# Performance work log

Hardware: AMD Instinct MI355X
Metric: run time of the kernel (lower is better)

## Reference

```python
import jax, jax.numpy as jnp
import numpy as np

B, N, G = 32, 262144, 256


def setup_inputs() -> dict:
    key = jax.random.key(0)
    k1, k2, k3 = jax.random.split(key, 3)
    pr = jax.random.normal(k1, (B, N), dtype=jnp.float32)
    inp_means = jax.random.normal(k2, (B, G), dtype=jnp.float32)
    vr = jax.random.randint(k3, (B, N, 1), 0, G, dtype=jnp.int32)
    W = jnp.ones((2,), dtype=jnp.float32)  # hist_weight, ones initializer
    return {"pr": pr, "inp_means": inp_means, "vr": vr, "W": W}


def reference(pr, inp_means, vr, W):
    sg = jax.lax.stop_gradient
    G = inp_means.shape[1]
    v = jnp.squeeze(vr, -1)  # [B, N] int cluster ids (stop_gradient in orig; int anyway)
    p_sg = sg(pr)

    # Per-batch segmented min/max/sum/any over clusters (replaces python loop over g).
    def seg(p, psg, vi):
        mn = jnp.full((G,), jnp.inf, p.dtype).at[vi].min(psg)    # min(where(gidx, pr, inf))
        mx = jnp.full((G,), -jnp.inf, p.dtype).at[vi].max(psg)   # max(where(gidx, pr, -inf))
        sm = jnp.zeros((G,), p.dtype).at[vi].add(p)              # sum(where(gidx, pr, 0))
        any_ = jnp.zeros((G,), bool).at[vi].set(True)            # reduce_any(gidx)
        return mn, mx, sm, any_

    vmins, vmaxs, vsum, vany = jax.vmap(seg)(pr, p_sg, v)  # each [B, G]
    # Original divides sum by cast(any)->1.0 (or 0/0=nan -> 0), i.e. the group SUM.
    vmeans = jnp.where(vany, vsum, jnp.zeros((), pr.dtype))
    vmeans = (inp_means * W[0] + vmeans * W[1]) / (W[0] + W[1])

    no_scale = vmins == vmaxs  # [B, G]
    vmins_g = jnp.take_along_axis(jnp.where(no_scale, 0.0, vmins), v, axis=1)  # [B, N]
    vmaxs_g = jnp.take_along_axis(jnp.where(no_scale, 1.0, vmaxs), v, axis=1)  # [B, N]

    sort_ids = jnp.argsort(vmeans, axis=1)
    orig_ids = jnp.argsort(sort_ids, axis=1)  # inverse permutation
    vs = jnp.take_along_axis(vmeans, sort_ids, axis=1)  # [B, G]
    cd = jnp.concatenate([vs[:, :1], vs, vs[:, -1:] * 2], axis=1)  # [B, G+2]
    # conv1d with kernel ones(2)/c, VALID: out[i] = (cd[i] + cd[i+1]) / c
    f0 = (cd[:, :-2] + cd[:, 1:-1]) / 1.999  # conv(...)[:, :-1]
    f1 = (cd[:, 1:-1] + cd[:, 2:]) / 2.001   # conv(...)[:, 1:]
    f0 = jnp.take_along_axis(
        jnp.where(no_scale, 0.0, jnp.take_along_axis(f0, orig_ids, axis=1)), v, axis=1)
    f1 = jnp.take_along_axis(
        jnp.where(no_scale, 1.0, jnp.take_along_axis(f1, orig_ids, axis=1)), v, axis=1)

    tmp = (sg(pr) - sg(vmins_g)) / sg(vmaxs_g - vmins_g) * (f1 - f0) + f0  # [B, N]
    bad = jnp.isnan(tmp) | (tmp == 0.0)
    s = pr / jnp.where(bad, 1.0, tmp)  # safe denominator (grad-safe)
    scale = jnp.where(bad | jnp.isnan(s) | jnp.isinf(s), 0.0, s)
    return pr * scale
```

## Files before the change

kernel.cpp:

```cpp
#include <hip/hip_runtime.h>
#include <math.h>

#define NB 32
#define NN 262144
#define NG 256
#define NC 64
#define CH (NN/NC)
#define SC (CH/4)
#define CD 64
#define ELD (NN/CD)

__global__ __launch_bounds__(256) void k_count(const int* __restrict__ vr,
                                               unsigned long long* __restrict__ wcnt16,
                                               unsigned* __restrict__ gid32){
  __shared__ unsigned sc[4][NG];
  const int t    = threadIdx.x;
  const int lane = t & 63;
  const int w    = t >> 6;
  sc[0][t] = 0u; sc[1][t] = 0u; sc[2][t] = 0u; sc[3][t] = 0u;
  __syncthreads();

  const int b = blockIdx.x / NC;
  const int c = blockIdx.x % NC;
  const size_t base = (size_t)b*NN + (size_t)c*CH;
  const int4* v4 = (const int4*)(vr + base);

#pragma unroll
  for (int i = 0; i < 4; i++){
    int idx = w*256 + i*64 + lane;
    int4 v = v4[idx];
    atomicAdd(&sc[w][v.x], 1u);
    atomicAdd(&sc[w][v.y], 1u);
    atomicAdd(&sc[w][v.z], 1u);
    atomicAdd(&sc[w][v.w], 1u);
    gid32[(base >> 2) + idx] =
      (unsigned)v.x | ((unsigned)v.y << 8) | ((unsigned)v.z << 16) | ((unsigned)v.w << 24);
  }
  __syncthreads();

  unsigned c0 = sc[0][t], c1 = sc[1][t], c2 = sc[2][t], c3 = sc[3][t];
  const size_t cb = (size_t)b*NC + c;
  wcnt16[cb*NG + t] = (unsigned long long)c0
                    | ((unsigned long long)c1 << 16)
                    | ((unsigned long long)c2 << 32)
                    | ((unsigned long long)c3 << 48);
}

__global__ __launch_bounds__(256) void k_offsets(const unsigned long long* __restrict__ wcnt16,
                                                 unsigned* __restrict__ off,
                                                 unsigned* __restrict__ grpbase,
                                                 unsigned* __restrict__ grplen){
  const int b = blockIdx.x;
  const int g = threadIdx.x;

  unsigned v[NC];
#pragma unroll
  for (int c = 0; c < NC; c++){
    unsigned long long x = wcnt16[(size_t)(b*NC + c)*NG + g];
    unsigned lo = (unsigned)x, hi = (unsigned)(x >> 32);
    v[c] = (lo & 0xFFFFu) + (lo >> 16) + (hi & 0xFFFFu) + (hi >> 16);
  }
  unsigned tot = 0;
#pragma unroll
  for (int c = 0; c < NC; c++) tot += v[c];

  __shared__ unsigned ss[NG];
  ss[g] = tot; __syncthreads();
  for (int d = 1; d < NG; d <<= 1){
    unsigned x = (g >= d) ? ss[g - d] : 0u;
    __syncthreads();
    ss[g] += x;
    __syncthreads();
  }
  unsigned base = ss[g] - tot;

  unsigned run = base;
#pragma unroll
  for (int c = 0; c < NC; c++){
    off[(size_t)(b*NC + c)*NG + g] = run;
    run += v[c];
  }
  grpbase[b*NG + g] = base;
  grplen [b*NG + g] = tot;
}

__global__ __launch_bounds__(256) void k_scatter(const float* __restrict__ pr,
                                                 const unsigned* __restrict__ gid32,
                                                 const unsigned* __restrict__ off,
                                                 const unsigned long long* __restrict__ wcnt16,
                                                 float* __restrict__ sorted){
  __shared__ float vbuf[CH];
  __shared__ unsigned char gbuf[CH];
  __shared__ unsigned wcnt[4][NG];
  __shared__ unsigned bias[NG];
  __shared__ unsigned wsum[4];
  const int t    = threadIdx.x;
  const int lane = t & 63;
  const int w    = t >> 6;
  const int b = blockIdx.x / NC;
  const int c = blockIdx.x % NC;
  const size_t base = (size_t)b*NN + (size_t)c*CH;
  const size_t cb   = (size_t)b*NC + c;

  {
    unsigned long long x = wcnt16[cb*NG + t];
    unsigned offt = off[cb*NG + t];
    unsigned lo = (unsigned)x, hi = (unsigned)(x >> 32);
    unsigned w0 = lo & 0xFFFFu, w1 = lo >> 16, w2 = hi & 0xFFFFu, w3 = hi >> 16;
    unsigned tot = w0 + w1 + w2 + w3;

    unsigned v = tot;
#pragma unroll
    for (int d = 1; d < 64; d <<= 1){
      unsigned y = __shfl_up(v, d, 64);
      if (lane >= d) v += y;
    }
    if (lane == 63) wsum[w] = v;
    __syncthreads();
    unsigned pre = 0;
#pragma unroll
    for (int k = 0; k < 3; k++) if (k < w) pre += wsum[k];
    unsigned lb = pre + v - tot;
    wcnt[0][t] = lb;
    wcnt[1][t] = lb + w0;
    wcnt[2][t] = lb + w0 + w1;
    wcnt[3][t] = lb + w0 + w1 + w2;
    bias[t] = offt - lb;
  }
  __syncthreads();

  {
    const unsigned long long below = (lane == 0) ? 0ull : ((1ull << lane) - 1ull);
    const float*    psrc = pr    + base        + (size_t)w*SC;
    const unsigned* gsrc = gid32 + (base >> 2) + (size_t)w*(SC/4);
    const int shft = (lane & 3) * 8;

    float pv[16]; unsigned pk[16];
#pragma unroll
    for (int s = 0; s < 16; s++){
      pv[s] = psrc[s*64 + lane];
      pk[s] = gsrc[s*16 + (lane >> 2)];
    }
#pragma unroll
    for (int s = 0; s < 16; s++){
      int g = (int)((pk[s] >> shft) & 255u);
      unsigned long long mask = ~0ull;
#pragma unroll
      for (int bit = 0; bit < 8; bit++){
        int bv = (g >> bit) & 1;
        unsigned long long bal = __ballot(bv);
        mask &= bv ? bal : ~bal;
      }
      int rank = __popcll(mask & below);
      unsigned old = wcnt[w][g];
      if (rank == 0) wcnt[w][g] = old + (unsigned)__popcll(mask);
      vbuf[old + (unsigned)rank] = pv[s];
      gbuf[old + (unsigned)rank] = (unsigned char)g;
    }
  }
  __syncthreads();

  {
    float* dst = sorted + (size_t)b*NN;
    const unsigned* gbuf32 = (const unsigned*)gbuf;
#pragma unroll
    for (int k = 0; k < CH/256; k++){
      int p = k*256 + t;
      unsigned packed = gbuf32[p >> 2];
      unsigned g = (packed >> ((p & 3) * 8)) & 255u;
      dst[bias[g] + (unsigned)p] = vbuf[p];
    }
  }
}

__global__ __launch_bounds__(32) void k_sum(const float* __restrict__ sorted,
                                            const unsigned* __restrict__ grpbase,
                                            const unsigned* __restrict__ grplen,
                                            float* __restrict__ gsum,
                                            float* __restrict__ gmn,
                                            float* __restrict__ gmx){
  const int lane = threadIdx.x;
  const int b = blockIdx.x >> 3;
  const int g = ((blockIdx.x & 7) << 5) + lane;

  const unsigned base = grpbase[b*NG + g];
  const unsigned len  = grplen [b*NG + g];
  const float* sp = sorted + (size_t)b*NN + base;

  float s = 0.0f, mn = INFINITY, mx = -INFINITY;

  unsigned head = (4u - ((unsigned)(((size_t)sp) >> 2) & 3u)) & 3u;
  if (head > len) head = len;
  for (unsigned i = 0; i < head; i++){
    float v = sp[i];
    s = __fadd_rn(s, v); mn = fminf(mn, v); mx = fmaxf(mx, v);
  }
  const float4* f4 = (const float4*)(sp + head);
  const unsigned rem   = len - head;
  const unsigned nfull = rem >> 4;

  float4 b0[4], b1[4], b2[4], b3[4], b4[4], b5[4], b6[4], b7[4];
#define LOADV(D, K) { D[0]=f4[(K)*4+0]; D[1]=f4[(K)*4+1]; D[2]=f4[(K)*4+2]; D[3]=f4[(K)*4+3]; }
#define CONS1(V)    { s=__fadd_rn(s,(V)); mn=fminf(mn,(V)); mx=fmaxf(mx,(V)); }
#define CONSV(D)    { _Pragma("unroll") for (int j = 0; j < 4; j++){ float4 q = D[j]; \
                      CONS1(q.x) CONS1(q.y) CONS1(q.z) CONS1(q.w) } }

  if (nfull > 0) LOADV(b0, 0)
  if (nfull > 1) LOADV(b1, 1)
  if (nfull > 2) LOADV(b2, 2)
  if (nfull > 3) LOADV(b3, 3)
  if (nfull > 4) LOADV(b4, 4)
  if (nfull > 5) LOADV(b5, 5)
  if (nfull > 6) LOADV(b6, 6)
  if (nfull > 7) LOADV(b7, 7)
  unsigned k = 0;
  for (; k + 8 <= nfull; k += 8){
    CONSV(b0) if (k +  8 < nfull) LOADV(b0, k +  8)
    CONSV(b1) if (k +  9 < nfull) LOADV(b1, k +  9)
    CONSV(b2) if (k + 10 < nfull) LOADV(b2, k + 10)
    CONSV(b3) if (k + 11 < nfull) LOADV(b3, k + 11)
    CONSV(b4) if (k + 12 < nfull) LOADV(b4, k + 12)
    CONSV(b5) if (k + 13 < nfull) LOADV(b5, k + 13)
    CONSV(b6) if (k + 14 < nfull) LOADV(b6, k + 14)
    CONSV(b7) if (k + 15 < nfull) LOADV(b7, k + 15)
  }
  {
    unsigned r = nfull - k;
    if (r > 0) CONSV(b0)
    if (r > 1) CONSV(b1)
    if (r > 2) CONSV(b2)
    if (r > 3) CONSV(b3)
    if (r > 4) CONSV(b4)
    if (r > 5) CONSV(b5)
    if (r > 6) CONSV(b6)
  }
  for (unsigned i = head + (nfull << 4); i < len; i++){
    float v = sp[i];
    s = __fadd_rn(s, v); mn = fminf(mn, v); mx = fmaxf(mx, v);
  }
#undef LOADV
#undef CONS1
#undef CONSV

  gsum[b*NG + g] = s;
  gmn [b*NG + g] = mn;
  gmx [b*NG + g] = mx;
}

__global__ __launch_bounds__(256) void k_pipeline(const float* __restrict__ gsum,
                                                  const float* __restrict__ gmn,
                                                  const float* __restrict__ gmx,
                                                  const float* __restrict__ inp_means,
                                                  const float* __restrict__ Wv,
                                                  float* __restrict__ params){
  const int b = blockIdx.x;
  const int g = threadIdx.x;
  __shared__ float vm[NG];
  __shared__ float vs[NG];

  const float s   = gsum[b*NG + g];
  const float mnf = gmn [b*NG + g];
  const float mxf = gmx [b*NG + g];
  const float W0 = Wv[0], W1 = Wv[1];
  float mean = __fdiv_rn(__fadd_rn(__fmul_rn(inp_means[b*NG + g], W0),
                                   __fmul_rn(s, W1)),
                         __fadd_rn(W0, W1));
  vm[g] = mean;
  __syncthreads();

  int r = 0;
  for (int j = 0; j < NG; j++){
    float x = vm[j];
    r += (x < mean) || (x == mean && j < g);
  }
  vs[r] = mean;
  __syncthreads();

  float c0 = (r == 0)    ? vs[0]                     : vs[r-1];
  float c1 = vs[r];
  float c2 = (r == NG-1) ? __fmul_rn(vs[NG-1], 2.0f) : vs[r+1];
  float f0 = __fdiv_rn(__fadd_rn(c0, c1), 1.999f);
  float f1 = __fdiv_rn(__fadd_rn(c1, c2), 2.001f);

  bool ns = (mnf == mxf);
  params[(b*4 + 0)*NG + g] = ns ? 0.0f : mnf;
  params[(b*4 + 1)*NG + g] = ns ? 1.0f : __fsub_rn(mxf, mnf);
  params[(b*4 + 2)*NG + g] = ns ? 1.0f : __fsub_rn(f1, f0);
  params[(b*4 + 3)*NG + g] = ns ? 0.0f : f0;
}

static __device__ __forceinline__ float apply_one(float p, unsigned g,
                                                  const float* __restrict__ sp0,
                                                  const float* __restrict__ sp1,
                                                  const float* __restrict__ sp2,
                                                  const float* __restrict__ sp3){
  float t1  = __fsub_rn(p, sp0[g]);
  float t3  = __fdiv_rn(t1, sp1[g]);
  float t5  = __fmul_rn(t3, sp2[g]);
  float tmp = __fadd_rn(t5, sp3[g]);
  bool bad = __builtin_isnan(tmp) || (tmp == 0.0f);
  float s = __fdiv_rn(p, bad ? 1.0f : tmp);
  bool bad2 = bad || __builtin_isnan(s) || __builtin_isinf(s);
  float sc = bad2 ? 0.0f : s;
  return __fmul_rn(p, sc);
}

__global__ __launch_bounds__(256) void k_apply(const float* __restrict__ pr,
                                               const unsigned* __restrict__ gid32,
                                               const float* __restrict__ params,
                                               float* __restrict__ out){
  __shared__ float sp0[NG], sp1[NG], sp2[NG], sp3[NG];
  const int t = threadIdx.x;
  const int b = blockIdx.x / CD;
  const int c = blockIdx.x % CD;

  sp0[t] = params[(b*4 + 0)*NG + t];
  sp1[t] = params[(b*4 + 1)*NG + t];
  sp2[t] = params[(b*4 + 2)*NG + t];
  sp3[t] = params[(b*4 + 3)*NG + t];
  __syncthreads();

  const size_t base = (size_t)b*NN + (size_t)c*ELD;
  const float4* p4 = (const float4*)(pr + base);
  float4* o4 = (float4*)(out + base);

#pragma unroll
  for (int i = 0; i < ELD/1024; i++){
    float4 p = p4[i*256 + t];
    unsigned pk = gid32[(base >> 2) + i*256 + t];
    float4 r;
    r.x = apply_one(p.x,  pk        & 255u, sp0, sp1, sp2, sp3);
    r.y = apply_one(p.y, (pk >>  8) & 255u, sp0, sp1, sp2, sp3);
    r.z = apply_one(p.z, (pk >> 16) & 255u, sp0, sp1, sp2, sp3);
    r.w = apply_one(p.w,  pk >> 24,         sp0, sp1, sp2, sp3);
    o4[i*256 + t] = r;
  }
}

extern "C" void kernel_launch(void* const* d_in, const int* in_sizes, int n_in,
                              void* d_out, int out_size, void* d_ws, size_t ws_size,
                              hipStream_t stream){
  const float* pr        = (const float*)d_in[0];
  const float* inp_means = (const float*)d_in[1];
  const int*   vr        = (const int*)d_in[2];
  const float* W         = (const float*)d_in[3];
  float* out = (float*)d_out;

  char* ws = (char*)d_ws;
  size_t o = 0;
  unsigned long long* wcnt16 = (unsigned long long*)(ws + o); o += (size_t)NB*NC*NG*8;
  unsigned* off     = (unsigned*)(ws + o); o += (size_t)NB*NC*NG*4;
  unsigned* gid32   = (unsigned*)(ws + o); o += (size_t)NB*NN;
  unsigned* grpbase = (unsigned*)(ws + o); o += (size_t)NB*NG*4;
  unsigned* grplen  = (unsigned*)(ws + o); o += (size_t)NB*NG*4;
  float*    gsum    = (float*)   (ws + o); o += (size_t)NB*NG*4;
  float*    gmn     = (float*)   (ws + o); o += (size_t)NB*NG*4;
  float*    gmx     = (float*)   (ws + o); o += (size_t)NB*NG*4;
  float*    params  = (float*)   (ws + o); o += (size_t)NB*NG*16;
  float* sorted = out;

  k_count   <<<NB*NC, 256, 0, stream>>>(vr, wcnt16, gid32);
  k_offsets <<<NB,     NG, 0, stream>>>(wcnt16, off, grpbase, grplen);
  k_scatter <<<NB*NC, 256, 0, stream>>>(pr, gid32, off, wcnt16, sorted);
  k_sum     <<<NB*8,   32, 0, stream>>>(sorted, grpbase, grplen, gsum, gmn, gmx);
  k_pipeline<<<NB,     NG, 0, stream>>>(gsum, gmn, gmx, inp_means, W, params);
  k_apply   <<<NB*CD, 256, 0, stream>>>(pr, gid32, params, out);
}
```

Measured before the change: 173.0 us.

## Double chunk count, wave-shuffle scan in offsets, derive group bounds from offsets

Doubles the number of chunks per batch, so the count and scatter kernels launch twice as many blocks, each holding half the data and a smaller shared buffer. k_offsets drops the 64-entry register array and the shared-memory Hillis-Steele scan. It uses a wavefront shuffle scan and re-reads the counts on the second pass. k_sum now derives group base and length from the first chunk's offsets, so the grpbase/grplen arrays go away. The price is twice the per-chunk count and offset traffic and twice the length of the serial loop over chunks in k_offsets.

```diff
diff --git a/kernel.cpp b/kernel.cpp
--- a/kernel.cpp
+++ b/kernel.cpp
@@ -4,15 +4,15 @@
 #define NB 32
 #define NN 262144
 #define NG 256
-#define NC 64
+#define NC 128
 #define CH (NN/NC)
 #define SC (CH/4)
 #define CD 64
 #define ELD (NN/CD)
 
-__global__ __launch_bounds__(256) void k_count(const int* __restrict__ vr,
-                                               unsigned long long* __restrict__ wcnt16,
-                                               unsigned* __restrict__ gid32){
+__global__ __launch_bounds__(256, 8) void k_count(const int* __restrict__ vr,
+                                                  unsigned long long* __restrict__ wcnt16,
+                                                  unsigned* __restrict__ gid32){
   __shared__ unsigned sc[4][NG];
   const int t    = threadIdx.x;
   const int lane = t & 63;
@@ -26,8 +26,8 @@
   const int4* v4 = (const int4*)(vr + base);
 
 #pragma unroll
-  for (int i = 0; i < 4; i++){
-    int idx = w*256 + i*64 + lane;
+  for (int i = 0; i < 2; i++){
+    int idx = w*128 + i*64 + lane;
     int4 v = v4[idx];
     atomicAdd(&sc[w][v.x], 1u);
     atomicAdd(&sc[w][v.y], 1u);
@@ -47,48 +47,50 @@
 }
 
 __global__ __launch_bounds__(256) void k_offsets(const unsigned long long* __restrict__ wcnt16,
-                                                 unsigned* __restrict__ off,
-                                                 unsigned* __restrict__ grpbase,
-                                                 unsigned* __restrict__ grplen){
+                                                 unsigned* __restrict__ off){
   const int b = blockIdx.x;
   const int g = threadIdx.x;
-
-  unsigned v[NC];
-#pragma unroll
+  const int lane = g & 63;
+  const int w    = g >> 6;
+  __shared__ unsigned wsum[4];
+
+  const unsigned long long* src = wcnt16 + (size_t)b*NC*NG + g;
+  unsigned tot = 0;
+#pragma unroll 8
   for (int c = 0; c < NC; c++){
-    unsigned long long x = wcnt16[(size_t)(b*NC + c)*NG + g];
+    unsigned long long x = src[(size_t)c*NG];
     unsigned lo = (unsigned)x, hi = (unsigned)(x >> 32);
-    v[c] = (lo & 0xFFFFu) + (lo >> 16) + (hi & 0xFFFFu) + (hi >> 16);
-  }
-  unsigned tot = 0;
-#pragma unroll
-  for (int c = 0; c < NC; c++) tot += v[c];
-
-  __shared__ unsigned ss[NG];
-  ss[g] = tot; __syncthreads();
-  for (int d = 1; d < NG; d <<= 1){
-    unsigned x = (g >= d) ? ss[g - d] : 0u;
-    __syncthreads();
-    ss[g] += x;
-    __syncthreads();
-  }
-  unsigned base = ss[g] - tot;
-
-  unsigned run = base;
-#pragma unroll
+    tot += (lo & 0xFFFFu) + (lo >> 16) + (hi & 0xFFFFu) + (hi >> 16);
+  }
+
+  unsigned vscan = tot;
+#pragma unroll
+  for (int d = 1; d < 64; d <<= 1){
+    unsigned y = __shfl_up(vscan, d, 64);
+    if (lane >= d) vscan += y;
+  }
+  if (lane == 63) wsum[w] = vscan;
+  __syncthreads();
+  unsigned pre = 0;
+#pragma unroll
+  for (int k = 0; k < 3; k++) if (k < w) pre += wsum[k];
+
+  unsigned run = pre + vscan - tot;
+  unsigned* dst = off + (size_t)b*NC*NG + g;
+#pragma unroll 8
   for (int c = 0; c < NC; c++){
-    off[(size_t)(b*NC + c)*NG + g] = run;
-    run += v[c];
-  }
-  grpbase[b*NG + g] = base;
-  grplen [b*NG + g] = tot;
-}
-
-__global__ __launch_bounds__(256) void k_scatter(const float* __restrict__ pr,
-                                                 const unsigned* __restrict__ gid32,
-                                                 const unsigned* __restrict__ off,
-                                                 const unsigned long long* __restrict__ wcnt16,
-                                                 float* __restrict__ sorted){
+    dst[(size_t)c*NG] = run;
+    unsigned long long x = src[(size_t)c*NG];
+    unsigned lo = (unsigned)x, hi = (unsigned)(x >> 32);
+    run += (lo & 0xFFFFu) + (lo >> 16) + (hi & 0xFFFFu) + (hi >> 16);
+  }
+}
+
+__global__ __launch_bounds__(256, 8) void k_scatter(const float* __restrict__ pr,
+                                                    const unsigned* __restrict__ gid32,
+                                                    const unsigned* __restrict__ off,
+                                                    const unsigned long long* __restrict__ wcnt16,
+                                                    float* __restrict__ sorted){
   __shared__ float vbuf[CH];
   __shared__ unsigned char gbuf[CH];
   __shared__ unsigned wcnt[4][NG];
@@ -135,14 +137,14 @@
     const unsigned* gsrc = gid32 + (base >> 2) + (size_t)w*(SC/4);
     const int shft = (lane & 3) * 8;
 
-    float pv[16]; unsigned pk[16];
-#pragma unroll
-    for (int s = 0; s < 16; s++){
+    float pv[8]; unsigned pk[8];
+#pragma unroll
+    for (int s = 0; s < 8; s++){
       pv[s] = psrc[s*64 + lane];
       pk[s] = gsrc[s*16 + (lane >> 2)];
     }
 #pragma unroll
-    for (int s = 0; s < 16; s++){
+    for (int s = 0; s < 8; s++){
       int g = (int)((pk[s] >> shft) & 255u);
       unsigned long long mask = ~0ull;
 #pragma unroll
@@ -174,8 +176,7 @@
 }
 
 __global__ __launch_bounds__(32) void k_sum(const float* __restrict__ sorted,
-                                            const unsigned* __restrict__ grpbase,
-                                            const unsigned* __restrict__ grplen,
+                                            const unsigned* __restrict__ off,
                                             float* __restrict__ gsum,
                                             float* __restrict__ gmn,
                                             float* __restrict__ gmx){
@@ -183,8 +184,10 @@
   const int b = blockIdx.x >> 3;
   const int g = ((blockIdx.x & 7) << 5) + lane;
 
-  const unsigned base = grpbase[b*NG + g];
-  const unsigned len  = grplen [b*NG + g];
+  const unsigned* ob = off + (size_t)b*NC*NG;
+  const unsigned base = ob[g];
+  const unsigned nxt  = (g == NG-1) ? (unsigned)NN : ob[g + 1];
+  const unsigned len  = nxt - base;
   const float* sp = sorted + (size_t)b*NN + base;
 
   float s = 0.0f, mn = INFINITY, mx = -INFINITY;
@@ -305,10 +308,10 @@
   return __fmul_rn(p, sc);
 }
 
-__global__ __launch_bounds__(256) void k_apply(const float* __restrict__ pr,
-                                               const unsigned* __restrict__ gid32,
-                                               const float* __restrict__ params,
-                                               float* __restrict__ out){
+__global__ __launch_bounds__(256, 8) void k_apply(const float* __restrict__ pr,
+                                                  const unsigned* __restrict__ gid32,
+                                                  const float* __restrict__ params,
+                                                  float* __restrict__ out){
   __shared__ float sp0[NG], sp1[NG], sp2[NG], sp3[NG];
   const int t = threadIdx.x;
   const int b = blockIdx.x / CD;
@@ -351,8 +354,6 @@
   unsigned long long* wcnt16 = (unsigned long long*)(ws + o); o += (size_t)NB*NC*NG*8;
   unsigned* off     = (unsigned*)(ws + o); o += (size_t)NB*NC*NG*4;
   unsigned* gid32   = (unsigned*)(ws + o); o += (size_t)NB*NN;
-  unsigned* grpbase = (unsigned*)(ws + o); o += (size_t)NB*NG*4;
-  unsigned* grplen  = (unsigned*)(ws + o); o += (size_t)NB*NG*4;
   float*    gsum    = (float*)   (ws + o); o += (size_t)NB*NG*4;
   float*    gmn     = (float*)   (ws + o); o += (size_t)NB*NG*4;
   float*    gmx     = (float*)   (ws + o); o += (size_t)NB*NG*4;
@@ -360,9 +361,9 @@
   float* sorted = out;
 
   k_count   <<<NB*NC, 256, 0, stream>>>(vr, wcnt16, gid32);
-  k_offsets <<<NB,     NG, 0, stream>>>(wcnt16, off, grpbase, grplen);
+  k_offsets <<<NB,    256, 0, stream>>>(wcnt16, off);
   k_scatter <<<NB*NC, 256, 0, stream>>>(pr, gid32, off, wcnt16, sorted);
-  k_sum     <<<NB*8,   32, 0, stream>>>(sorted, grpbase, grplen, gsum, gmn, gmx);
-  k_pipeline<<<NB,     NG, 0, stream>>>(gsum, gmn, gmx, inp_means, W, params);
+  k_sum     <<<NB*8,   32, 0, stream>>>(sorted, off, gsum, gmn, gmx);
+  k_pipeline<<<NB,    256, 0, stream>>>(gsum, gmn, gmx, inp_means, W, params);
   k_apply   <<<NB*CD, 256, 0, stream>>>(pr, gid32, params, out);
 }
```

New measurement: 177.7 us. 2.7% more time.

## Fuse offset prefix computation into scatter kernel, dropping k_offsets launch

Applied to the files above, without the earlier changes.

Removes the separate k_offsets kernel. Each scatter block now reads all 64 chunk counts for its batch, computes per-group totals and the prefix of earlier chunks itself, and derives its global offsets. This saves one kernel launch and the round trip of the off array through memory. In exchange, every scatter block does redundant reads of the batch count table (64x256 64-bit words per block), which should mostly hit L2.

```diff
diff --git a/kernel.cpp b/kernel.cpp
--- a/kernel.cpp
+++ b/kernel.cpp
@@ -46,86 +46,65 @@
                     | ((unsigned long long)c3 << 48);
 }
 
-__global__ __launch_bounds__(256) void k_offsets(const unsigned long long* __restrict__ wcnt16,
-                                                 unsigned* __restrict__ off,
+__global__ __launch_bounds__(256) void k_scatter(const float* __restrict__ pr,
+                                                 const unsigned* __restrict__ gid32,
+                                                 const unsigned long long* __restrict__ wcnt16,
+                                                 float* __restrict__ sorted,
                                                  unsigned* __restrict__ grpbase,
                                                  unsigned* __restrict__ grplen){
-  const int b = blockIdx.x;
-  const int g = threadIdx.x;
-
-  unsigned v[NC];
-#pragma unroll
-  for (int c = 0; c < NC; c++){
-    unsigned long long x = wcnt16[(size_t)(b*NC + c)*NG + g];
-    unsigned lo = (unsigned)x, hi = (unsigned)(x >> 32);
-    v[c] = (lo & 0xFFFFu) + (lo >> 16) + (hi & 0xFFFFu) + (hi >> 16);
-  }
-  unsigned tot = 0;
-#pragma unroll
-  for (int c = 0; c < NC; c++) tot += v[c];
-
-  __shared__ unsigned ss[NG];
-  ss[g] = tot; __syncthreads();
-  for (int d = 1; d < NG; d <<= 1){
-    unsigned x = (g >= d) ? ss[g - d] : 0u;
-    __syncthreads();
-    ss[g] += x;
-    __syncthreads();
-  }
-  unsigned base = ss[g] - tot;
-
-  unsigned run = base;
-#pragma unroll
-  for (int c = 0; c < NC; c++){
-    off[(size_t)(b*NC + c)*NG + g] = run;
-    run += v[c];
-  }
-  grpbase[b*NG + g] = base;
-  grplen [b*NG + g] = tot;
-}
-
-__global__ __launch_bounds__(256) void k_scatter(const float* __restrict__ pr,
-                                                 const unsigned* __restrict__ gid32,
-                                                 const unsigned* __restrict__ off,
-                                                 const unsigned long long* __restrict__ wcnt16,
-                                                 float* __restrict__ sorted){
   __shared__ float vbuf[CH];
   __shared__ unsigned char gbuf[CH];
   __shared__ unsigned wcnt[4][NG];
   __shared__ unsigned bias[NG];
-  __shared__ unsigned wsum[4];
+  __shared__ unsigned wsumA[4];
+  __shared__ unsigned wsumO[4];
   const int t    = threadIdx.x;
   const int lane = t & 63;
   const int w    = t >> 6;
   const int b = blockIdx.x / NC;
   const int c = blockIdx.x % NC;
   const size_t base = (size_t)b*NN + (size_t)c*CH;
-  const size_t cb   = (size_t)b*NC + c;
 
   {
-    unsigned long long x = wcnt16[cb*NG + t];
-    unsigned offt = off[cb*NG + t];
-    unsigned lo = (unsigned)x, hi = (unsigned)(x >> 32);
+    const unsigned long long* tab = wcnt16 + (size_t)b*NC*NG + t;
+    unsigned long long own = 0;
+    unsigned tot_all = 0, tot_before = 0;
+#pragma unroll 8
+    for (int cc = 0; cc < NC; cc++){
+      unsigned long long x = tab[(size_t)cc*NG];
+      unsigned lo = (unsigned)x, hi = (unsigned)(x >> 32);
+      unsigned tt = (lo & 0xFFFFu) + (lo >> 16) + (hi & 0xFFFFu) + (hi >> 16);
+      tot_all += tt;
+      if (cc < c)  tot_before += tt;
+      if (cc == c) own = x;
+    }
+    unsigned lo = (unsigned)own, hi = (unsigned)(own >> 32);
     unsigned w0 = lo & 0xFFFFu, w1 = lo >> 16, w2 = hi & 0xFFFFu, w3 = hi >> 16;
-    unsigned tot = w0 + w1 + w2 + w3;
-
-    unsigned v = tot;
+    unsigned tot_own = w0 + w1 + w2 + w3;
+
+    unsigned va = tot_all, vo = tot_own;
 #pragma unroll
     for (int d = 1; d < 64; d <<= 1){
-      unsigned y = __shfl_up(v, d, 64);
-      if (lane >= d) v += y;
-    }
-    if (lane == 63) wsum[w] = v;
+      unsigned ya = __shfl_up(va, d, 64);
+      unsigned yo = __shfl_up(vo, d, 64);
+      if (lane >= d){ va += ya; vo += yo; }
+    }
+    if (lane == 63){ wsumA[w] = va; wsumO[w] = vo; }
     __syncthreads();
-    unsigned pre = 0;
-#pragma unroll
-    for (int k = 0; k < 3; k++) if (k < w) pre += wsum[k];
-    unsigned lb = pre + v - tot;
+    unsigned preA = 0, preO = 0;
+#pragma unroll
+    for (int k = 0; k < 3; k++) if (k < w){ preA += wsumA[k]; preO += wsumO[k]; }
+    unsigned base_g = preA + va - tot_all;
+    unsigned lb     = preO + vo - tot_own;
     wcnt[0][t] = lb;
     wcnt[1][t] = lb + w0;
     wcnt[2][t] = lb + w0 + w1;
     wcnt[3][t] = lb + w0 + w1 + w2;
-    bias[t] = offt - lb;
+    bias[t] = (base_g + tot_before) - lb;
+    if (c == 0){
+      grpbase[b*NG + t] = base_g;
+      grplen [b*NG + t] = tot_all;
+    }
   }
   __syncthreads();
 
@@ -349,7 +328,6 @@
   char* ws = (char*)d_ws;
   size_t o = 0;
   unsigned long long* wcnt16 = (unsigned long long*)(ws + o); o += (size_t)NB*NC*NG*8;
-  unsigned* off     = (unsigned*)(ws + o); o += (size_t)NB*NC*NG*4;
   unsigned* gid32   = (unsigned*)(ws + o); o += (size_t)NB*NN;
   unsigned* grpbase = (unsigned*)(ws + o); o += (size_t)NB*NG*4;
   unsigned* grplen  = (unsigned*)(ws + o); o += (size_t)NB*NG*4;
@@ -360,9 +338,8 @@
   float* sorted = out;
 
   k_count   <<<NB*NC, 256, 0, stream>>>(vr, wcnt16, gid32);
-  k_offsets <<<NB,     NG, 0, stream>>>(wcnt16, off, grpbase, grplen);
-  k_scatter <<<NB*NC, 256, 0, stream>>>(pr, gid32, off, wcnt16, sorted);
+  k_scatter <<<NB*NC, 256, 0, stream>>>(pr, gid32, wcnt16, sorted, grpbase, grplen);
   k_sum     <<<NB*8,   32, 0, stream>>>(sorted, grpbase, grplen, gsum, gmn, gmx);
-  k_pipeline<<<NB,     NG, 0, stream>>>(gsum, gmn, gmx, inp_means, W, params);
+  k_pipeline<<<NB,    256, 0, stream>>>(gsum, gmn, gmx, inp_means, W, params);
   k_apply   <<<NB*CD, 256, 0, stream>>>(pr, gid32, params, out);
 }
```

Result: no change. 173.3 us (+0.2%).
